# Optimization experiments

Hardware: AMD Instinct MI355X
Metric: run time of the kernel (lower is better)

The kernel has to match this reference:

```python
import jax, jax.numpy as jnp
from jax import lax
import numpy as np

B, C, S, H, DH, DV, DW = 16, 256, 64, 8, 32, 32, 32  # batch, channels, input_size, heads, d_h, d_v, d_w


def _dwconv(x, w, b):
    # depthwise 3x3 conv, stride 1, pad 1. w: [C,1,3,3]
    y = lax.conv_general_dilated(x, w, (1, 1), ((1, 1), (1, 1)),
                                 dimension_numbers=('NCHW', 'OIHW', 'NCHW'),
                                 feature_group_count=x.shape[1])
    return y + b[None, :, None, None]


def _linear(x, w, b):
    # torch Linear: w [out,in]
    return x @ w.T + b


def setup_inputs() -> dict:
    key = jax.random.key(0)
    ks = jax.random.split(key, 26)
    n = lambda k, shape, s=0.02: jax.random.normal(k, shape, jnp.float32) * s
    conv = lambda k: n(k, (C, 1, 3, 3), 0.1)
    return {
        'x': jax.random.normal(ks[0], (B, C, S, S), jnp.float32),
        'dw_qh_w': conv(ks[1]), 'dw_qh_b': n(ks[2], (C,)),
        'fc_qh_w': n(ks[3], (H * DH, C)), 'fc_qh_b': n(ks[4], (H * DH,)),
        'dw_kh_w': conv(ks[5]), 'dw_kh_b': n(ks[6], (C,)),
        'fc_kh_w': n(ks[7], (H * DH, C)), 'fc_kh_b': n(ks[8], (H * DH,)),
        'Bh': n(ks[9], (1, H, S, S)),
        'dw_v_w': conv(ks[10]), 'dw_v_b': n(ks[11], (C,)),
        'fc_v_w': n(ks[12], (H * DV, C)), 'fc_v_b': n(ks[13], (H * DV,)),
        'dw_qw_w': conv(ks[14]), 'dw_qw_b': n(ks[15], (C,)),
        'fc_qw_w': n(ks[16], (H * DW, C)), 'fc_qw_b': n(ks[17], (H * DW,)),
        'dw_kw_w': conv(ks[18]), 'dw_kw_b': n(ks[19], (C,)),
        'fc_kw_w': n(ks[20], (H * DW, C)), 'fc_kw_b': n(ks[21], (H * DW,)),
        'Bw': n(ks[22], (1, H, S, S)),
        'fc_o_w': n(ks[23], (C, H * DV)), 'fc_o_b': n(ks[24], (C,)),
    }


def reference(x, dw_qh_w, dw_qh_b, fc_qh_w, fc_qh_b,
              dw_kh_w, dw_kh_b, fc_kh_w, fc_kh_b, Bh,
              dw_v_w, dw_v_b, fc_v_w, fc_v_b,
              dw_qw_w, dw_qw_b, fc_qw_w, fc_qw_b,
              dw_kw_w, dw_kw_b, fc_kw_w, fc_kw_b, Bw,
              fc_o_w, fc_o_b):
    b, c, h, w = x.shape
    sh = DH ** -0.5
    sw = DW ** -0.5

    # height-axis queries/keys: dwconv -> adaptive avg pool over width -> linear
    qh = _dwconv(x, dw_qh_w, dw_qh_b).mean(axis=3).transpose(0, 2, 1)  # [b,h,c]
    qh = _linear(qh, fc_qh_w, fc_qh_b).reshape(b, h, H, DH).transpose(0, 2, 1, 3)  # [b,H,h,dh]
    kh = _dwconv(x, dw_kh_w, dw_kh_b).mean(axis=3).transpose(0, 2, 1)
    kh = _linear(kh, fc_kh_w, fc_kh_b).reshape(b, h, H, DH).transpose(0, 2, 1, 3)
    attn_h = jax.nn.softmax(jnp.einsum('bhid,bhjd->bhij', qh, kh) * sh + Bh, axis=-1)  # [b,H,h,h]

    # values over full HxW grid
    v = _dwconv(x, dw_v_w, dw_v_b).reshape(b, c, h * w).transpose(0, 2, 1)  # [b,hw,c]
    v = _linear(v, fc_v_w, fc_v_b).reshape(b, h, w, H, DV).transpose(0, 3, 1, 2, 4)  # [b,H,h,w,dv]
    v = v.reshape(b, H, h, w * DV)

    # width-axis queries/keys: dwconv -> adaptive avg pool over height -> linear
    qw = _dwconv(x, dw_qw_w, dw_qw_b).mean(axis=2).transpose(0, 2, 1)  # [b,w,c]
    qw = _linear(qw, fc_qw_w, fc_qw_b).reshape(b, w, H, DW).transpose(0, 2, 1, 3)  # [b,H,w,dw]
    kw = _dwconv(x, dw_kw_w, dw_kw_b).mean(axis=2).transpose(0, 2, 1)
    kw = _linear(kw, fc_kw_w, fc_kw_b).reshape(b, w, H, DW).transpose(0, 2, 1, 3)
    attn_w = jax.nn.softmax(jnp.einsum('bhid,bhjd->bhij', qw, kw) * sw + Bw, axis=-1)  # [b,H,w,w]

    # dual axial mixing: height attention, then width attention
    r = jnp.matmul(attn_h, v)                                # [b,H,h,w*dv]
    r = r.reshape(b, H, h, w, DV).transpose(0, 1, 2, 4, 3)    # [b,H,h,dv,w]
    r = r.reshape(b, H, h * DV, w)
    r = jnp.matmul(r, attn_w)                                # [b,H,h*dv,w]
    r = r.reshape(b, H, h, DV, w).transpose(0, 2, 4, 1, 3)    # [b,h,w,H,dv]
    r = r.reshape(b, h * w, H * DV)
    out = _linear(r, fc_o_w, fc_o_b).reshape(b, C, h, w)      # faithful to torch .view
    return out
```

## Files before the change

### kernel.cpp

```cpp
#include <hip/hip_runtime.h>
#include <hip/hip_bf16.h>

typedef float f4v __attribute__((ext_vector_type(4)));
typedef short s8v __attribute__((ext_vector_type(8)));
typedef unsigned short u8v __attribute__((ext_vector_type(8)));

__device__ __forceinline__ float bf2f(ushort u) {
  union { unsigned int i; float f; } c; c.i = ((unsigned int)u) << 16;
  return c.f;
}
__device__ __forceinline__ ushort f2bf(float f) {
  union { ushort s; __hip_bfloat16 h; } c; c.h = __float2bfloat16(f);
  return c.s;
}
__device__ __forceinline__ void gload16(const ushort* g, ushort* l) {
  __builtin_amdgcn_global_load_lds(
      (const __attribute__((address_space(1))) unsigned int*)g,
      (__attribute__((address_space(3))) unsigned int*)l, 16, 0, 0);
}

__global__ __launch_bounds__(256) void k_conv(
    const float* __restrict__ x,
    const float* __restrict__ wqh, const float* __restrict__ bqh,
    const float* __restrict__ wkh, const float* __restrict__ bkh,
    const float* __restrict__ wv,  const float* __restrict__ bv,
    const float* __restrict__ wqw, const float* __restrict__ bqw,
    const float* __restrict__ wkw, const float* __restrict__ bkw,
    const float* __restrict__ fq0, const float* __restrict__ fq1,
    const float* __restrict__ fq2, const float* __restrict__ fq3,
    const float* __restrict__ fwv, const float* __restrict__ fwo,
    ushort* __restrict__ whl, ushort* __restrict__ wbf,
    ushort* __restrict__ convV,
    float* __restrict__ qhm, float* __restrict__ khm,
    float* __restrict__ qwm, float* __restrict__ kwm) {
  __shared__ float xs[68 * 68];
  __shared__ float wl[5][9];
  __shared__ float bl[5];

  int bx = blockIdx.x;
  int tid = threadIdx.x;

  if (bx >= 4096) {
    int pb = bx - 4096;
    if (pb < 1024) {
      int mat = pb >> 8;
      int i = (pb & 255) * 256 + tid;
      const float* p = mat == 0 ? fq0 : mat == 1 ? fq1 : mat == 2 ? fq2 : fq3;
      float f = p[i];
      ushort hi = f2bf(f);
      ushort lo = f2bf(f - bf2f(hi));
      whl[(size_t)mat * 131072 + i] = hi;
      whl[(size_t)mat * 131072 + 65536 + i] = lo;
    } else {
      int idx = (pb - 1024) * 256 + tid;
      const float* src = (idx >> 16) ? fwo : fwv;
      wbf[idx] = f2bf(src[idx & 65535]);
    }
    return;
  }

  int b = bx >> 8;
  int c = bx & 255;
  int lane = tid & 63, wave = tid >> 6;

  const float* xp = x + (size_t)(b * 256 + c) * 4096;
#pragma unroll
  for (int i = 0; i < 4; i++) {
    int flat = tid + i * 256;
    int r = flat >> 4, c4 = (flat & 15) * 4;
    float4 v = *(const float4*)(xp + r * 64 + c4);
    *(float4*)&xs[(r + 1) * 68 + 4 + c4] = v;
  }
  if (tid < 72) { xs[tid] = 0.f; xs[65 * 68 + tid] = 0.f; }
  if (tid >= 72 && tid < 200) {
    int t = tid - 72;
    int pr = (t & 63) + 1, side = t >> 6;
    xs[pr * 68 + (side ? 68 : 3)] = 0.f;
  }
  if (tid >= 200 && tid < 245) {
    int t = tid - 200;
    int cw = t / 9, wi = t % 9;
    const float* wp = cw == 0 ? wqh : cw == 1 ? wkh : cw == 2 ? wv
                    : cw == 3 ? wqw : wkw;
    wl[cw][wi] = wp[c * 9 + wi];
  } else if (tid >= 245 && tid < 250) {
    int cw = tid - 245;
    const float* bp = cw == 0 ? bqh : cw == 1 ? bkh : cw == 2 ? bv
                    : cw == 3 ? bqw : bkw;
    bl[cw] = bp[c];
  }
  __syncthreads();

  {
    int w = lane;
    int h0 = wave * 16;
    float v0 = wl[2][0], v1 = wl[2][1], v2 = wl[2][2];
    float v3 = wl[2][3], v4 = wl[2][4], v5 = wl[2][5];
    float v6 = wl[2][6], v7 = wl[2][7], v8 = wl[2][8];
    float bvv = bl[2];
    float a00 = xs[h0 * 68 + 3 + w], a01 = xs[h0 * 68 + 4 + w],
          a02 = xs[h0 * 68 + 5 + w];
    float a10 = xs[(h0 + 1) * 68 + 3 + w], a11 = xs[(h0 + 1) * 68 + 4 + w],
          a12 = xs[(h0 + 1) * 68 + 5 + w];
    ushort* cp = convV + (size_t)(b * 256 + c) * 4096 + h0 * 64 + w;
#pragma unroll
    for (int i = 0; i < 16; i++) {
      int pr = h0 + i + 2;
      float a20 = xs[pr * 68 + 3 + w];
      float a21 = xs[pr * 68 + 4 + w];
      float a22 = xs[pr * 68 + 5 + w];
      float acc = bvv;
      acc += a00 * v0 + a01 * v1 + a02 * v2;
      acc += a10 * v3 + a11 * v4 + a12 * v5;
      acc += a20 * v6 + a21 * v7 + a22 * v8;
      cp[i * 64] = f2bf(acc);
      a00 = a10; a01 = a11; a02 = a12;
      a10 = a20; a11 = a21; a12 = a22;
    }
  }

  if (wave == 0) {
    float rs = 0.f, e0 = 0.f, e1 = 0.f;
    const float* rowp = &xs[(lane + 1) * 68 + 4];
#pragma unroll
    for (int i = 0; i < 16; i++) {
      float4 v = *(const float4*)(rowp + i * 4);
      rs += (v.x + v.y) + (v.z + v.w);
      if (i == 0) e0 = v.x;
      if (i == 15) e1 = v.w;
    }
    float rsP = __shfl(rs, lane - 1, 64); rsP = (lane == 0) ? 0.f : rsP;
    float rsN = __shfl(rs, lane + 1, 64); rsN = (lane == 63) ? 0.f : rsN;
    float e0P = __shfl(e0, lane - 1, 64); e0P = (lane == 0) ? 0.f : e0P;
    float e0N = __shfl(e0, lane + 1, 64); e0N = (lane == 63) ? 0.f : e0N;
    float e1P = __shfl(e1, lane - 1, 64); e1P = (lane == 0) ? 0.f : e1P;
    float e1N = __shfl(e1, lane + 1, 64); e1N = (lane == 63) ? 0.f : e1N;
    float RS[3] = {rsP, rs, rsN};
    float E0[3] = {e0P, e0, e0N};
    float E1[3] = {e1P, e1, e1N};
    float vq = 0.f, vk = 0.f;
#pragma unroll
    for (int ky = 0; ky < 3; ky++) {
      vq += (wl[0][ky * 3] + wl[0][ky * 3 + 1] + wl[0][ky * 3 + 2]) * RS[ky]
            - wl[0][ky * 3] * E1[ky] - wl[0][ky * 3 + 2] * E0[ky];
      vk += (wl[1][ky * 3] + wl[1][ky * 3 + 1] + wl[1][ky * 3 + 2]) * RS[ky]
            - wl[1][ky * 3] * E1[ky] - wl[1][ky * 3 + 2] * E0[ky];
    }
    qhm[(size_t)(b * 256 + c) * 64 + lane] = vq * (1.f / 64.f) + bl[0];
    khm[(size_t)(b * 256 + c) * 64 + lane] = vk * (1.f / 64.f) + bl[1];
  } else if (wave == 1) {
    float cs = 0.f, f0 = 0.f, f1 = 0.f;
#pragma unroll
    for (int r = 0; r < 64; r++) {
      float v = xs[(r + 1) * 68 + 4 + lane];
      cs += v;
      if (r == 0) f0 = v;
      if (r == 63) f1 = v;
    }
    float csP = __shfl(cs, lane - 1, 64); csP = (lane == 0) ? 0.f : csP;
    float csN = __shfl(cs, lane + 1, 64); csN = (lane == 63) ? 0.f : csN;
    float f0P = __shfl(f0, lane - 1, 64); f0P = (lane == 0) ? 0.f : f0P;
    float f0N = __shfl(f0, lane + 1, 64); f0N = (lane == 63) ? 0.f : f0N;
    float f1P = __shfl(f1, lane - 1, 64); f1P = (lane == 0) ? 0.f : f1P;
    float f1N = __shfl(f1, lane + 1, 64); f1N = (lane == 63) ? 0.f : f1N;
    float CS[3] = {csP, cs, csN};
    float F0[3] = {f0P, f0, f0N};
    float F1[3] = {f1P, f1, f1N};
    float vq = 0.f, vk = 0.f;
#pragma unroll
    for (int kx = 0; kx < 3; kx++) {
      vq += (wl[3][kx] + wl[3][3 + kx] + wl[3][6 + kx]) * CS[kx]
            - wl[3][kx] * F1[kx] - wl[3][6 + kx] * F0[kx];
      vk += (wl[4][kx] + wl[4][3 + kx] + wl[4][6 + kx]) * CS[kx]
            - wl[4][kx] * F1[kx] - wl[4][6 + kx] * F0[kx];
    }
    qwm[(size_t)(b * 256 + c) * 64 + lane] = vq * (1.f / 64.f) + bl[3];
    kwm[(size_t)(b * 256 + c) * 64 + lane] = vk * (1.f / 64.f) + bl[4];
  }
}

__global__ __launch_bounds__(256) void k_mmv(
    const ushort* __restrict__ A, const ushort* __restrict__ W,
    const float* __restrict__ bias, ushort* __restrict__ out,
    const float* __restrict__ s0, const float* __restrict__ s1,
    const float* __restrict__ s2, const float* __restrict__ s3,
    const ushort* __restrict__ whl,
    const float* __restrict__ b0, const float* __restrict__ b1,
    const float* __restrict__ b2, const float* __restrict__ b3,
    float* __restrict__ d0, float* __restrict__ d1,
    float* __restrict__ d2, float* __restrict__ d3) {
  __shared__ __align__(16) ushort pool[17408];

  int bx = blockIdx.x;
  int tid = threadIdx.x;
  int lane = tid & 63, wave = tid >> 6;
  int tm = lane & 15, quad = lane >> 4;

  if (bx < 512) {
    ushort* As = pool;
    ushort* Bs = pool + 4096;

    int m0 = bx * 128;
    int wm = (wave & 1) * 64, wn = (wave >> 1) * 128;
    int xorv = (tm ^ (tm >> 2)) & 3;
    int srow = lane >> 2;
    int slot = lane & 3;

    const ushort* Abase = A + (size_t)(m0 >> 12) * (256 * 4096) + (m0 & 4095);

    f4v acc[4][8] = {};

    for (int kc = 0; kc < 256; kc += 32) {
      __syncthreads();
      {
        int kr2 = (tid & 15) * 2, mg = tid >> 4;
        u8v v0 = *(const u8v*)&Abase[(size_t)(kc + kr2) * 4096 + mg * 8];
        u8v v1 = *(const u8v*)&Abase[(size_t)(kc + kr2 + 1) * 4096 + mg * 8];
        int sl0 = kr2 >> 3, k7 = kr2 & 7;
#pragma unroll
        for (int j = 0; j < 8; j++) {
          int row = mg * 8 + j;
          int xr = (row ^ (row >> 2)) & 3;
          ushort pr[2] = {v0[j], v1[j]};
          *(uint*)&As[row * 32 + (sl0 ^ xr) * 8 + k7] = *(uint*)pr;
        }
      }
#pragma unroll
      for (int it = 0; it < 4; it++) {
        int rb = wave * 16 + it * 64;
        int row = rb + srow;
        int xr = (row ^ (row >> 2)) & 3;
        gload16(&W[(size_t)row * 256 + kc + (slot ^ xr) * 8], &Bs[rb * 32]);
      }
      __syncthreads();

      s8v a[4];
#pragma unroll
      for (int mi = 0; mi < 4; mi++)
        a[mi] = *(const s8v*)&As[(wm + mi * 16 + tm) * 32 + (quad ^ xorv) * 8];
#pragma unroll
      for (int ni = 0; ni < 8; ni++) {
        s8v bfr =
            *(const s8v*)&Bs[(wn + ni * 16 + tm) * 32 + (quad ^ xorv) * 8];
#pragma unroll
        for (int mi = 0; mi < 4; mi++)
          acc[mi][ni] = __builtin_amdgcn_mfma_f32_16x16x32_bf16(
              a[mi], bfr, acc[mi][ni], 0, 0, 0);
      }
    }

#pragma unroll
    for (int mi = 0; mi < 4; mi++) {
#pragma unroll
      for (int ni = 0; ni < 8; ni++) {
        int col = wn + ni * 16 + tm;
        float bv = bias[col];
#pragma unroll
        for (int r = 0; r < 4; r++) {
          int row = m0 + wm + mi * 16 + quad * 4 + r;
          out[(size_t)row * 256 + col] = f2bf(acc[mi][ni][r] + bv);
        }
      }
    }
    return;
  }

  {
    int t = bx - 512;
    int z = t & 3;
    int n0 = ((t >> 2) & 3) * 64;
    int b = t >> 4;

    ushort* Ah = pool;
    ushort* Al = pool + 4352;
    ushort* Wh = pool + 8704;
    ushort* Wl = pool + 13056;

    const float* At = z == 0 ? s0 : z == 1 ? s1 : z == 2 ? s2 : s3;
    const ushort* Whp = whl + (size_t)z * 131072;
    const ushort* Wlp = Whp + 65536;
    const float* biasz = z == 0 ? b0 : z == 1 ? b1 : z == 2 ? b2 : b3;
    float* Cout = z == 0 ? d0 : z == 1 ? d1 : z == 2 ? d2 : d3;

    const float* Ab = At + (size_t)b * 256 * 64;

    int wm = (wave & 1) * 32, wn = (wave >> 1) * 32;

    f4v acc[2][2] = {};

    for (int kc = 0; kc < 256; kc += 64) {
      __syncthreads();
#pragma unroll
      for (int t2 = 0; t2 < 2; t2++) {
        int task = tid + t2 * 256;
        int mq = task & 15, kp = task >> 4;
        int k0 = kp * 2, m0 = mq * 4;
        float4 v0 = *(const float4*)&Ab[(size_t)(kc + k0) * 64 + m0];
        float4 v1 = *(const float4*)&Ab[(size_t)(kc + k0 + 1) * 64 + m0];
        float f0[4] = {v0.x, v0.y, v0.z, v0.w};
        float f1[4] = {v1.x, v1.y, v1.z, v1.w};
#pragma unroll
        for (int j = 0; j < 4; j++) {
          ushort h0 = f2bf(f0[j]), h1 = f2bf(f1[j]);
          ushort l0 = f2bf(f0[j] - bf2f(h0)), l1 = f2bf(f1[j] - bf2f(h1));
          ushort ph[2] = {h0, h1};
          ushort pl[2] = {l0, l1};
          *(uint*)&Ah[(m0 + j) * 68 + k0] = *(uint*)ph;
          *(uint*)&Al[(m0 + j) * 68 + k0] = *(uint*)pl;
        }
      }
#pragma unroll
      for (int t2 = 0; t2 < 2; t2++) {
        int task = tid + t2 * 256;
        int nr = task >> 3, k8 = (task & 7) * 8;
        *(u8v*)&Wh[nr * 68 + k8] =
            *(const u8v*)&Whp[(size_t)(n0 + nr) * 256 + kc + k8];
        *(u8v*)&Wl[nr * 68 + k8] =
            *(const u8v*)&Wlp[(size_t)(n0 + nr) * 256 + kc + k8];
      }
      __syncthreads();

#pragma unroll
      for (int ks = 0; ks < 64; ks += 32) {
        s8v ah[2], al[2], bh[2], bl[2];
#pragma unroll
        for (int mi = 0; mi < 2; mi++) {
          int idx = (wm + mi * 16 + tm) * 68 + ks + quad * 8;
          union { s8v v; unsigned long long u[2]; } th, tl;
          th.u[0] = *(const unsigned long long*)&Ah[idx];
          th.u[1] = *(const unsigned long long*)&Ah[idx + 4];
          tl.u[0] = *(const unsigned long long*)&Al[idx];
          tl.u[1] = *(const unsigned long long*)&Al[idx + 4];
          ah[mi] = th.v;
          al[mi] = tl.v;
        }
#pragma unroll
        for (int ni = 0; ni < 2; ni++) {
          int idx = (wn + ni * 16 + tm) * 68 + ks + quad * 8;
          union { s8v v; unsigned long long u[2]; } th, tl;
          th.u[0] = *(const unsigned long long*)&Wh[idx];
          th.u[1] = *(const unsigned long long*)&Wh[idx + 4];
          tl.u[0] = *(const unsigned long long*)&Wl[idx];
          tl.u[1] = *(const unsigned long long*)&Wl[idx + 4];
          bh[ni] = th.v;
          bl[ni] = tl.v;
        }
#pragma unroll
        for (int mi = 0; mi < 2; mi++)
#pragma unroll
          for (int ni = 0; ni < 2; ni++) {
            acc[mi][ni] = __builtin_amdgcn_mfma_f32_16x16x32_bf16(
                ah[mi], bh[ni], acc[mi][ni], 0, 0, 0);
            acc[mi][ni] = __builtin_amdgcn_mfma_f32_16x16x32_bf16(
                ah[mi], bl[ni], acc[mi][ni], 0, 0, 0);
            acc[mi][ni] = __builtin_amdgcn_mfma_f32_16x16x32_bf16(
                al[mi], bh[ni], acc[mi][ni], 0, 0, 0);
          }
      }
    }

#pragma unroll
    for (int mi = 0; mi < 2; mi++) {
#pragma unroll
      for (int ni = 0; ni < 2; ni++) {
        int n = n0 + wn + ni * 16 + tm;
        float bv = biasz[n];
#pragma unroll
        for (int r = 0; r < 4; r++) {
          int m = b * 64 + wm + mi * 16 + quad * 4 + r;
          Cout[(size_t)m * 256 + n] = acc[mi][ni][r] + bv;
        }
      }
    }
  }
}

template <int OUT_BF16, int AT>
__global__ __launch_bounds__(256) void k_mm(const ushort* __restrict__ A,
                                            const ushort* __restrict__ W,
                                            const float* __restrict__ bias,
                                            void* __restrict__ out) {
  __shared__ __align__(16) ushort As[128 * 32];
  __shared__ __align__(16) ushort Bs[128 * 32];

  int m0 = blockIdx.x * 128;
  int n0 = blockIdx.y * 128;
  int tid = threadIdx.x;
  int lane = tid & 63, wave = tid >> 6;
  int wm = (wave & 1) * 64, wn = (wave >> 1) * 64;
  int tm = lane & 15, quad = lane >> 4;
  int xorv = (tm ^ (tm >> 2)) & 3;
  int srow = lane >> 2;
  int slot = lane & 3;

  const ushort* Abase;
  if (AT) {
    Abase = A + (size_t)(m0 >> 12) * (256 * 4096) + (m0 & 4095);
  } else {
    Abase = A + (size_t)m0 * 256;
  }

  f4v acc[4][4] = {};

  for (int kc = 0; kc < 256; kc += 32) {
    __syncthreads();
    if (AT) {
      int kr2 = (tid & 15) * 2, mg = tid >> 4;
      u8v v0 = *(const u8v*)&Abase[(size_t)(kc + kr2) * 4096 + mg * 8];
      u8v v1 = *(const u8v*)&Abase[(size_t)(kc + kr2 + 1) * 4096 + mg * 8];
      int sl0 = kr2 >> 3, k7 = kr2 & 7;
#pragma unroll
      for (int j = 0; j < 8; j++) {
        int row = mg * 8 + j;
        int xr = (row ^ (row >> 2)) & 3;
        ushort pr[2] = {v0[j], v1[j]};
        *(uint*)&As[row * 32 + (sl0 ^ xr) * 8 + k7] = *(uint*)pr;
      }
#pragma unroll
      for (int it = 0; it < 2; it++) {
        int rb = wave * 16 + it * 64;
        int row = rb + srow;
        int xr = (row ^ (row >> 2)) & 3;
        gload16(&W[(size_t)(n0 + row) * 256 + kc + (slot ^ xr) * 8],
                &Bs[rb * 32]);
      }
    } else {
#pragma unroll
      for (int it = 0; it < 2; it++) {
        int rb = wave * 16 + it * 64;
        int row = rb + srow;
        int xr = (row ^ (row >> 2)) & 3;
        gload16(&Abase[(size_t)row * 256 + kc + (slot ^ xr) * 8],
                &As[rb * 32]);
        gload16(&W[(size_t)(n0 + row) * 256 + kc + (slot ^ xr) * 8],
                &Bs[rb * 32]);
      }
    }
    __syncthreads();

    s8v a[4], bfr[4];
#pragma unroll
    for (int mi = 0; mi < 4; mi++)
      a[mi] = *(const s8v*)&As[(wm + mi * 16 + tm) * 32 + (quad ^ xorv) * 8];
#pragma unroll
    for (int ni = 0; ni < 4; ni++)
      bfr[ni] = *(const s8v*)&Bs[(wn + ni * 16 + tm) * 32 + (quad ^ xorv) * 8];
#pragma unroll
    for (int mi = 0; mi < 4; mi++)
#pragma unroll
      for (int ni = 0; ni < 4; ni++)
        acc[mi][ni] = __builtin_amdgcn_mfma_f32_16x16x32_bf16(
            a[mi], bfr[ni], acc[mi][ni], 0, 0, 0);
  }

#pragma unroll
  for (int mi = 0; mi < 4; mi++) {
#pragma unroll
    for (int ni = 0; ni < 4; ni++) {
      int col = n0 + wn + ni * 16 + tm;
      float bv = bias[col];
#pragma unroll
      for (int r = 0; r < 4; r++) {
        int row = m0 + wm + mi * 16 + quad * 4 + r;
        float v = acc[mi][ni][r] + bv;
        if (OUT_BF16)
          ((ushort*)out)[(size_t)row * 256 + col] = f2bf(v);
        else
          ((float*)out)[(size_t)row * 256 + col] = v;
      }
    }
  }
}

__global__ __launch_bounds__(256) void k_attn(
    const float* __restrict__ qh, const float* __restrict__ kh,
    const float* __restrict__ Bh, float* __restrict__ ah,
    const float* __restrict__ qw, const float* __restrict__ kw,
    const float* __restrict__ Bw, float* __restrict__ aw, float scale) {
  __shared__ float qs[64 * 33];
  __shared__ float ks[64 * 33];

  int bx = blockIdx.x;
  int setw = bx >> 7;
  int rem = bx & 127;
  int hd = rem & 7, b = rem >> 3;
  int tid = threadIdx.x;
  int wave = tid >> 6, lane = tid & 63;

  const float* q = setw ? qw : qh;
  const float* k = setw ? kw : kh;
  const float* Bb = setw ? Bw : Bh;
  float* attn = setw ? aw : ah;

#pragma unroll
  for (int it = 0; it < 8; it++) {
    int f = tid + it * 256;
    int j = f >> 5, d = f & 31;
    size_t src = (size_t)(b * 64 + j) * 256 + hd * 32 + d;
    qs[j * 33 + d] = q[src];
    ks[j * 33 + d] = k[src];
  }
  __syncthreads();

  const float* Bp = Bb + (size_t)(hd * 64) * 64;
  float* ap = attn + (size_t)((b * 8 + hd) * 64) * 64;
  int j = lane;
  for (int ig = 0; ig < 16; ig++) {
    int i = ig * 4 + wave;
    float dot = 0.f;
#pragma unroll
    for (int d = 0; d < 32; d++) dot += qs[i * 33 + d] * ks[j * 33 + d];
    float logit = dot * scale + Bp[i * 64 + j];
    float mx = logit;
#pragma unroll
    for (int off = 32; off > 0; off >>= 1)
      mx = fmaxf(mx, __shfl_xor(mx, off, 64));
    float e = __expf(logit - mx);
    float sum = e;
#pragma unroll
    for (int off = 32; off > 0; off >>= 1) sum += __shfl_xor(sum, off, 64);
    ap[i * 64 + j] = e / sum;
  }
}

__global__ __launch_bounds__(256) void k_av(const float* __restrict__ attn,
                                            const ushort* __restrict__ vlin,
                                            ushort* __restrict__ r1) {
  __shared__ __align__(16) ushort Ah[64 * 68];
  __shared__ __align__(16) ushort Al[64 * 68];
  __shared__ __align__(16) ushort Bt[256 * 68];

  int bx = blockIdx.x;
  int nt = bx & 7, hd = (bx >> 3) & 7, b = bx >> 6;
  int n0 = nt * 256;
  int tid = threadIdx.x;
  int lane = tid & 63, wave = tid >> 6;

  const float* ap = attn + (size_t)(b * 8 + hd) * 4096;
  {
    int i = tid >> 2;
    int j0 = (tid & 3) * 16;
#pragma unroll
    for (int p = 0; p < 4; p++) {
      float4 v = *(const float4*)&ap[i * 64 + j0 + p * 4];
      float f_[4] = {v.x, v.y, v.z, v.w};
      ushort ph[4], pl[4];
#pragma unroll
      for (int q = 0; q < 4; q++) {
        ph[q] = f2bf(f_[q]);
        pl[q] = f2bf(f_[q] - bf2f(ph[q]));
      }
      *(uint2*)&Ah[i * 68 + j0 + p * 4] = *(uint2*)ph;
      *(uint2*)&Al[i * 68 + j0 + p * 4] = *(uint2*)pl;
    }
  }
  {
#pragma unroll
    for (int p = 0; p < 4; p++) {
      int task = tid + p * 256;
      int jp = task & 31;
      int cc = task >> 5;
      int j = jp * 2;
      int c = cc * 8;
      int gcol = n0 + c;
      int w = gcol >> 5, dv = gcol & 31;
      const ushort* vp =
          &vlin[(size_t)(b * 4096 + j * 64 + w) * 256 + hd * 32 + dv];
      u8v v0 = *(const u8v*)vp;
      u8v v1 = *(const u8v*)(vp + 64 * 256);
#pragma unroll
      for (int q = 0; q < 8; q++) {
        ushort pr[2] = {(ushort)v0[q], (ushort)v1[q]};
        *(uint*)&Bt[(c + q) * 68 + j] = *(uint*)pr;
      }
    }
  }
  __syncthreads();

  int tm = lane & 15, quad = lane >> 4;
  int wn = wave * 64;
  f4v acc[4][4] = {};
#pragma unroll
  for (int kc = 0; kc < 64; kc += 32) {
    s8v ah_[4], al_[4], bb[4];
#pragma unroll
    for (int mi = 0; mi < 4; mi++) {
      int idx = (mi * 16 + tm) * 68 + kc + quad * 8;
      union { s8v v; unsigned long long u[2]; } th, tl;
      th.u[0] = *(const unsigned long long*)&Ah[idx];
      th.u[1] = *(const unsigned long long*)&Ah[idx + 4];
      tl.u[0] = *(const unsigned long long*)&Al[idx];
      tl.u[1] = *(const unsigned long long*)&Al[idx + 4];
      ah_[mi] = th.v;
      al_[mi] = tl.v;
    }
#pragma unroll
    for (int ni = 0; ni < 4; ni++) {
      int idx = (wn + ni * 16 + tm) * 68 + kc + quad * 8;
      union { s8v v; unsigned long long u[2]; } tb;
      tb.u[0] = *(const unsigned long long*)&Bt[idx];
      tb.u[1] = *(const unsigned long long*)&Bt[idx + 4];
      bb[ni] = tb.v;
    }
#pragma unroll
    for (int mi = 0; mi < 4; mi++)
#pragma unroll
      for (int ni = 0; ni < 4; ni++) {
        acc[mi][ni] = __builtin_amdgcn_mfma_f32_16x16x32_bf16(
            ah_[mi], bb[ni], acc[mi][ni], 0, 0, 0);
        acc[mi][ni] = __builtin_amdgcn_mfma_f32_16x16x32_bf16(
            al_[mi], bb[ni], acc[mi][ni], 0, 0, 0);
      }
  }

  ushort* rp = r1 + (size_t)(b * 8 + hd) * 64 * 2048;
#pragma unroll
  for (int mi = 0; mi < 4; mi++) {
#pragma unroll
    for (int ni = 0; ni < 4; ni++) {
      int col = n0 + wn + ni * 16 + tm;
#pragma unroll
      for (int r = 0; r < 4; r++) {
        int row = mi * 16 + quad * 4 + r;
        rp[(size_t)row * 2048 + col] = f2bf(acc[mi][ni][r]);
      }
    }
  }
}

__global__ __launch_bounds__(256) void k_rw(const ushort* __restrict__ r1,
                                            const float* __restrict__ attnw,
                                            ushort* __restrict__ yT) {
  __shared__ __align__(16) ushort As[8 * 2180];
  __shared__ __align__(16) ushort Wh[64 * 68];
  __shared__ __align__(16) ushort Wl[64 * 68];

  int bx = blockIdx.x;
  int ht = bx & 7, hd = (bx >> 3) & 7, b = bx >> 6;
  int tid = threadIdx.x;
  int lane = tid & 63, wave = tid >> 6;

  {
    int h = tid >> 5;
    int t = tid & 31;
    const ushort* rp =
        r1 + (size_t)((b * 8 + hd) * 64 + ht * 8 + h) * 2048;
#pragma unroll
    for (int i = 0; i < 4; i++) {
      int chunk = t + 32 * i;
      int w = (chunk >> 2) * 2;
      int dv0 = (chunk & 3) * 8;
      u8v v0 = *(const u8v*)&rp[w * 32 + dv0];
      u8v v1 = *(const u8v*)&rp[(w + 1) * 32 + dv0];
#pragma unroll
      for (int j = 0; j < 8; j++) {
        ushort pr[2] = {(ushort)v0[j], (ushort)v1[j]};
        *(uint*)&As[h * 2180 + (dv0 + j) * 68 + w] = *(uint*)pr;
      }
    }
  }
  {
    const float* ap = attnw + (size_t)(b * 8 + hd) * 4096;
#pragma unroll
    for (int p = 0; p < 4; p++) {
      int w = (tid >> 4) + p * 16;
      int wq = (tid & 15) * 4;
      float4 v = *(const float4*)&ap[w * 64 + wq];
      float f_[4] = {v.x, v.y, v.z, v.w};
#pragma unroll
      for (int j = 0; j < 4; j++) {
        ushort hi = f2bf(f_[j]);
        Wh[(wq + j) * 68 + w] = hi;
        Wl[(wq + j) * 68 + w] = f2bf(f_[j] - bf2f(hi));
      }
    }
  }
  __syncthreads();

  int tm = lane & 15, quad = lane >> 4;
  int h0 = wave * 2;
  f4v acc[4][4] = {};
#pragma unroll
  for (int kc = 0; kc < 64; kc += 32) {
    s8v a[4], bh[4], bl[4];
#pragma unroll
    for (int mi = 0; mi < 4; mi++) {
      int h = h0 + (mi >> 1);
      int dv = (mi & 1) * 16 + tm;
      int idx = h * 2180 + dv * 68 + kc + quad * 8;
      union { s8v v; unsigned long long u[2]; } t_;
      t_.u[0] = *(const unsigned long long*)&As[idx];
      t_.u[1] = *(const unsigned long long*)&As[idx + 4];
      a[mi] = t_.v;
    }
#pragma unroll
    for (int ni = 0; ni < 4; ni++) {
      int idx = (ni * 16 + tm) * 68 + kc + quad * 8;
      union { s8v v; unsigned long long u[2]; } th, tl;
      th.u[0] = *(const unsigned long long*)&Wh[idx];
      th.u[1] = *(const unsigned long long*)&Wh[idx + 4];
      tl.u[0] = *(const unsigned long long*)&Wl[idx];
      tl.u[1] = *(const unsigned long long*)&Wl[idx + 4];
      bh[ni] = th.v;
      bl[ni] = tl.v;
    }
#pragma unroll
    for (int mi = 0; mi < 4; mi++)
#pragma unroll
      for (int ni = 0; ni < 4; ni++) {
        acc[mi][ni] = __builtin_amdgcn_mfma_f32_16x16x32_bf16(
            a[mi], bh[ni], acc[mi][ni], 0, 0, 0);
        acc[mi][ni] = __builtin_amdgcn_mfma_f32_16x16x32_bf16(
            a[mi], bl[ni], acc[mi][ni], 0, 0, 0);
      }
  }

#pragma unroll
  for (int mi = 0; mi < 4; mi++) {
    int h = ht * 8 + h0 + (mi >> 1);
    int dv0 = (mi & 1) * 16 + quad * 4;
#pragma unroll
    for (int ni = 0; ni < 4; ni++) {
      int wp = ni * 16 + tm;
      ushort pk[4];
#pragma unroll
      for (int r = 0; r < 4; r++) pk[r] = f2bf(acc[mi][ni][r]);
      *(uint2*)&yT[(size_t)(b * 4096 + h * 64 + wp) * 256 + hd * 32 + dv0] =
          *(uint2*)pk;
    }
  }
}

extern "C" void kernel_launch(void* const* d_in, const int* in_sizes, int n_in,
                              void* d_out, int out_size, void* d_ws,
                              size_t ws_size, hipStream_t stream) {
  const float* x      = (const float*)d_in[0];
  const float* dwqh_w = (const float*)d_in[1];
  const float* dwqh_b = (const float*)d_in[2];
  const float* fcqh_w = (const float*)d_in[3];
  const float* fcqh_b = (const float*)d_in[4];
  const float* dwkh_w = (const float*)d_in[5];
  const float* dwkh_b = (const float*)d_in[6];
  const float* fckh_w = (const float*)d_in[7];
  const float* fckh_b = (const float*)d_in[8];
  const float* Bh     = (const float*)d_in[9];
  const float* dwv_w  = (const float*)d_in[10];
  const float* dwv_b  = (const float*)d_in[11];
  const float* fcv_w  = (const float*)d_in[12];
  const float* fcv_b  = (const float*)d_in[13];
  const float* dwqw_w = (const float*)d_in[14];
  const float* dwqw_b = (const float*)d_in[15];
  const float* fcqw_w = (const float*)d_in[16];
  const float* fcqw_b = (const float*)d_in[17];
  const float* dwkw_w = (const float*)d_in[18];
  const float* dwkw_b = (const float*)d_in[19];
  const float* fckw_w = (const float*)d_in[20];
  const float* fckw_b = (const float*)d_in[21];
  const float* Bw     = (const float*)d_in[22];
  const float* fco_w  = (const float*)d_in[23];
  const float* fco_b  = (const float*)d_in[24];

  char* base = (char*)d_ws;
  ushort* P1 = (ushort*)(base);
  ushort* P2 = (ushort*)(base + 33554432);
  ushort* P3 = (ushort*)(base + 67108864);
  ushort* whl  = (ushort*)(base + 100663296);
  ushort* wv_bf = (ushort*)(base + 101711872);
  float* qhm = (float*)(base + 101974016);
  float* khm = qhm + 262144;
  float* qwm = khm + 262144;
  float* kwm = qwm + 262144;
  float* qhl = kwm + 262144;
  float* khl = qhl + 262144;
  float* qwl = khl + 262144;
  float* kwl = qwl + 262144;
  float* ah  = kwl + 262144;
  float* awt = ah + 524288;
  if (ws_size < 115000000ull) return;

  const float scale = 0.17677669529663687f;

  k_conv<<<5632, 256, 0, stream>>>(x, dwqh_w, dwqh_b, dwkh_w, dwkh_b, dwv_w,
                                   dwv_b, dwqw_w, dwqw_b, dwkw_w, dwkw_b,
                                   fcqh_w, fckh_w, fcqw_w, fckw_w, fcv_w,
                                   fco_w, whl, wv_bf, P1,
                                   qhm, khm, qwm, kwm);
  k_mmv<<<768, 256, 0, stream>>>(P1, wv_bf, fcv_b, P3,
                                 qhm, khm, qwm, kwm, whl, fcqh_b, fckh_b,
                                 fcqw_b, fckw_b, qhl, khl, qwl, kwl);
  k_attn<<<256, 256, 0, stream>>>(qhl, khl, Bh, ah, qwl, kwl, Bw, awt, scale);
  k_av<<<1024, 256, 0, stream>>>(ah, P3, P1);
  k_rw<<<1024, 256, 0, stream>>>(P1, awt, P2);
  k_mm<0, 0><<<dim3(512, 2), 256, 0, stream>>>(P2, wv_bf + 65536, fco_b, d_out);
}
```

Baseline: 273.1 us.

## Fuse attention softmax into AV and width-mix kernels; widen output GEMM tile

Removes the separate attention kernel and instead recomputes the 64x64 softmax attention maps inside each k_av and k_rw block, writing the hi/lo bf16 split directly to shared memory. This drops one launch and the global round trip of the attention matrices. In exchange, each of the 8 blocks per (batch, head) recomputes the same attention map redundantly. The output projection is also rewritten so each block covers all 256 output columns with a 128x256 tile, which halves the grid and reads the A tile once.

New measurement: 301.9 us. 10.5% more time.

```diff
diff --git a/kernel.cpp b/kernel.cpp
--- a/kernel.cpp
+++ b/kernel.cpp
@@ -375,157 +375,12 @@
   }
 }
 
-template <int OUT_BF16, int AT>
-__global__ __launch_bounds__(256) void k_mm(const ushort* __restrict__ A,
-                                            const ushort* __restrict__ W,
-                                            const float* __restrict__ bias,
-                                            void* __restrict__ out) {
-  __shared__ __align__(16) ushort As[128 * 32];
-  __shared__ __align__(16) ushort Bs[128 * 32];
-
-  int m0 = blockIdx.x * 128;
-  int n0 = blockIdx.y * 128;
-  int tid = threadIdx.x;
-  int lane = tid & 63, wave = tid >> 6;
-  int wm = (wave & 1) * 64, wn = (wave >> 1) * 64;
-  int tm = lane & 15, quad = lane >> 4;
-  int xorv = (tm ^ (tm >> 2)) & 3;
-  int srow = lane >> 2;
-  int slot = lane & 3;
-
-  const ushort* Abase;
-  if (AT) {
-    Abase = A + (size_t)(m0 >> 12) * (256 * 4096) + (m0 & 4095);
-  } else {
-    Abase = A + (size_t)m0 * 256;
-  }
-
-  f4v acc[4][4] = {};
-
-  for (int kc = 0; kc < 256; kc += 32) {
-    __syncthreads();
-    if (AT) {
-      int kr2 = (tid & 15) * 2, mg = tid >> 4;
-      u8v v0 = *(const u8v*)&Abase[(size_t)(kc + kr2) * 4096 + mg * 8];
-      u8v v1 = *(const u8v*)&Abase[(size_t)(kc + kr2 + 1) * 4096 + mg * 8];
-      int sl0 = kr2 >> 3, k7 = kr2 & 7;
-#pragma unroll
-      for (int j = 0; j < 8; j++) {
-        int row = mg * 8 + j;
-        int xr = (row ^ (row >> 2)) & 3;
-        ushort pr[2] = {v0[j], v1[j]};
-        *(uint*)&As[row * 32 + (sl0 ^ xr) * 8 + k7] = *(uint*)pr;
-      }
-#pragma unroll
-      for (int it = 0; it < 2; it++) {
-        int rb = wave * 16 + it * 64;
-        int row = rb + srow;
-        int xr = (row ^ (row >> 2)) & 3;
-        gload16(&W[(size_t)(n0 + row) * 256 + kc + (slot ^ xr) * 8],
-                &Bs[rb * 32]);
-      }
-    } else {
-#pragma unroll
-      for (int it = 0; it < 2; it++) {
-        int rb = wave * 16 + it * 64;
-        int row = rb + srow;
-        int xr = (row ^ (row >> 2)) & 3;
-        gload16(&Abase[(size_t)row * 256 + kc + (slot ^ xr) * 8],
-                &As[rb * 32]);
-        gload16(&W[(size_t)(n0 + row) * 256 + kc + (slot ^ xr) * 8],
-                &Bs[rb * 32]);
-      }
-    }
-    __syncthreads();
-
-    s8v a[4], bfr[4];
-#pragma unroll
-    for (int mi = 0; mi < 4; mi++)
-      a[mi] = *(const s8v*)&As[(wm + mi * 16 + tm) * 32 + (quad ^ xorv) * 8];
-#pragma unroll
-    for (int ni = 0; ni < 4; ni++)
-      bfr[ni] = *(const s8v*)&Bs[(wn + ni * 16 + tm) * 32 + (quad ^ xorv) * 8];
-#pragma unroll
-    for (int mi = 0; mi < 4; mi++)
-#pragma unroll
-      for (int ni = 0; ni < 4; ni++)
-        acc[mi][ni] = __builtin_amdgcn_mfma_f32_16x16x32_bf16(
-            a[mi], bfr[ni], acc[mi][ni], 0, 0, 0);
-  }
-
-#pragma unroll
-  for (int mi = 0; mi < 4; mi++) {
-#pragma unroll
-    for (int ni = 0; ni < 4; ni++) {
-      int col = n0 + wn + ni * 16 + tm;
-      float bv = bias[col];
-#pragma unroll
-      for (int r = 0; r < 4; r++) {
-        int row = m0 + wm + mi * 16 + quad * 4 + r;
-        float v = acc[mi][ni][r] + bv;
-        if (OUT_BF16)
-          ((ushort*)out)[(size_t)row * 256 + col] = f2bf(v);
-        else
-          ((float*)out)[(size_t)row * 256 + col] = v;
-      }
-    }
-  }
-}
-
-__global__ __launch_bounds__(256) void k_attn(
-    const float* __restrict__ qh, const float* __restrict__ kh,
-    const float* __restrict__ Bh, float* __restrict__ ah,
-    const float* __restrict__ qw, const float* __restrict__ kw,
-    const float* __restrict__ Bw, float* __restrict__ aw, float scale) {
-  __shared__ float qs[64 * 33];
-  __shared__ float ks[64 * 33];
-
-  int bx = blockIdx.x;
-  int setw = bx >> 7;
-  int rem = bx & 127;
-  int hd = rem & 7, b = rem >> 3;
-  int tid = threadIdx.x;
-  int wave = tid >> 6, lane = tid & 63;
-
-  const float* q = setw ? qw : qh;
-  const float* k = setw ? kw : kh;
-  const float* Bb = setw ? Bw : Bh;
-  float* attn = setw ? aw : ah;
-
-#pragma unroll
-  for (int it = 0; it < 8; it++) {
-    int f = tid + it * 256;
-    int j = f >> 5, d = f & 31;
-    size_t src = (size_t)(b * 64 + j) * 256 + hd * 32 + d;
-    qs[j * 33 + d] = q[src];
-    ks[j * 33 + d] = k[src];
-  }
-  __syncthreads();
-
-  const float* Bp = Bb + (size_t)(hd * 64) * 64;
-  float* ap = attn + (size_t)((b * 8 + hd) * 64) * 64;
-  int j = lane;
-  for (int ig = 0; ig < 16; ig++) {
-    int i = ig * 4 + wave;
-    float dot = 0.f;
-#pragma unroll
-    for (int d = 0; d < 32; d++) dot += qs[i * 33 + d] * ks[j * 33 + d];
-    float logit = dot * scale + Bp[i * 64 + j];
-    float mx = logit;
-#pragma unroll
-    for (int off = 32; off > 0; off >>= 1)
-      mx = fmaxf(mx, __shfl_xor(mx, off, 64));
-    float e = __expf(logit - mx);
-    float sum = e;
-#pragma unroll
-    for (int off = 32; off > 0; off >>= 1) sum += __shfl_xor(sum, off, 64);
-    ap[i * 64 + j] = e / sum;
-  }
-}
-
-__global__ __launch_bounds__(256) void k_av(const float* __restrict__ attn,
+__global__ __launch_bounds__(256) void k_av(const float* __restrict__ q,
+                                            const float* __restrict__ k,
+                                            const float* __restrict__ Bb,
                                             const ushort* __restrict__ vlin,
-                                            ushort* __restrict__ r1) {
+                                            ushort* __restrict__ r1,
+                                            float scale) {
   __shared__ __align__(16) ushort Ah[64 * 68];
   __shared__ __align__(16) ushort Al[64 * 68];
   __shared__ __align__(16) ushort Bt[256 * 68];
@@ -536,24 +391,42 @@
   int tid = threadIdx.x;
   int lane = tid & 63, wave = tid >> 6;
 
-  const float* ap = attn + (size_t)(b * 8 + hd) * 4096;
   {
-    int i = tid >> 2;
-    int j0 = (tid & 3) * 16;
-#pragma unroll
-    for (int p = 0; p < 4; p++) {
-      float4 v = *(const float4*)&ap[i * 64 + j0 + p * 4];
-      float f_[4] = {v.x, v.y, v.z, v.w};
-      ushort ph[4], pl[4];
-#pragma unroll
-      for (int q = 0; q < 4; q++) {
-        ph[q] = f2bf(f_[q]);
-        pl[q] = f2bf(f_[q] - bf2f(ph[q]));
-      }
-      *(uint2*)&Ah[i * 68 + j0 + p * 4] = *(uint2*)ph;
-      *(uint2*)&Al[i * 68 + j0 + p * 4] = *(uint2*)pl;
-    }
-  }
+    float* qs = (float*)Bt;
+    float* ks = qs + 64 * 33;
+#pragma unroll
+    for (int it = 0; it < 8; it++) {
+      int f = tid + it * 256;
+      int j = f >> 5, d = f & 31;
+      size_t src = (size_t)(b * 64 + j) * 256 + hd * 32 + d;
+      qs[j * 33 + d] = q[src];
+      ks[j * 33 + d] = k[src];
+    }
+    __syncthreads();
+    const float* Bp = Bb + (size_t)(hd * 64) * 64;
+    int j = lane;
+    for (int ig = 0; ig < 16; ig++) {
+      int i = ig * 4 + wave;
+      float dot = 0.f;
+#pragma unroll
+      for (int d = 0; d < 32; d++) dot += qs[i * 33 + d] * ks[j * 33 + d];
+      float logit = dot * scale + Bp[i * 64 + j];
+      float mx = logit;
+#pragma unroll
+      for (int off = 32; off > 0; off >>= 1)
+        mx = fmaxf(mx, __shfl_xor(mx, off, 64));
+      float e = __expf(logit - mx);
+      float sum = e;
+#pragma unroll
+      for (int off = 32; off > 0; off >>= 1) sum += __shfl_xor(sum, off, 64);
+      float a = e / sum;
+      ushort hi = f2bf(a);
+      Ah[i * 68 + j] = hi;
+      Al[i * 68 + j] = f2bf(a - bf2f(hi));
+    }
+    __syncthreads();
+  }
+
   {
 #pragma unroll
     for (int p = 0; p < 4; p++) {
@@ -569,9 +442,9 @@
       u8v v0 = *(const u8v*)vp;
       u8v v1 = *(const u8v*)(vp + 64 * 256);
 #pragma unroll
-      for (int q = 0; q < 8; q++) {
-        ushort pr[2] = {(ushort)v0[q], (ushort)v1[q]};
-        *(uint*)&Bt[(c + q) * 68 + j] = *(uint*)pr;
+      for (int qq = 0; qq < 8; qq++) {
+        ushort pr[2] = {(ushort)v0[qq], (ushort)v1[qq]};
+        *(uint*)&Bt[(c + qq) * 68 + j] = *(uint*)pr;
       }
     }
   }
@@ -629,8 +502,11 @@
 }
 
 __global__ __launch_bounds__(256) void k_rw(const ushort* __restrict__ r1,
-                                            const float* __restrict__ attnw,
-                                            ushort* __restrict__ yT) {
+                                            const float* __restrict__ q,
+                                            const float* __restrict__ k,
+                                            const float* __restrict__ Bb,
+                                            ushort* __restrict__ yT,
+                                            float scale) {
   __shared__ __align__(16) ushort As[8 * 2180];
   __shared__ __align__(16) ushort Wh[64 * 68];
   __shared__ __align__(16) ushort Wl[64 * 68];
@@ -639,6 +515,42 @@
   int ht = bx & 7, hd = (bx >> 3) & 7, b = bx >> 6;
   int tid = threadIdx.x;
   int lane = tid & 63, wave = tid >> 6;
+
+  {
+    float* qs = (float*)As;
+    float* ks = qs + 64 * 33;
+#pragma unroll
+    for (int it = 0; it < 8; it++) {
+      int f = tid + it * 256;
+      int j = f >> 5, d = f & 31;
+      size_t src = (size_t)(b * 64 + j) * 256 + hd * 32 + d;
+      qs[j * 33 + d] = q[src];
+      ks[j * 33 + d] = k[src];
+    }
+    __syncthreads();
+    const float* Bp = Bb + (size_t)(hd * 64) * 64;
+    int j = lane;
+    for (int ig = 0; ig < 16; ig++) {
+      int i = ig * 4 + wave;
+      float dot = 0.f;
+#pragma unroll
+      for (int d = 0; d < 32; d++) dot += qs[i * 33 + d] * ks[j * 33 + d];
+      float logit = dot * scale + Bp[i * 64 + j];
+      float mx = logit;
+#pragma unroll
+      for (int off = 32; off > 0; off >>= 1)
+        mx = fmaxf(mx, __shfl_xor(mx, off, 64));
+      float e = __expf(logit - mx);
+      float sum = e;
+#pragma unroll
+      for (int off = 32; off > 0; off >>= 1) sum += __shfl_xor(sum, off, 64);
+      float a = e / sum;
+      ushort hi = f2bf(a);
+      Wh[j * 68 + i] = hi;
+      Wl[j * 68 + i] = f2bf(a - bf2f(hi));
+    }
+    __syncthreads();
+  }
 
   {
     int h = tid >> 5;
@@ -656,22 +568,6 @@
       for (int j = 0; j < 8; j++) {
         ushort pr[2] = {(ushort)v0[j], (ushort)v1[j]};
         *(uint*)&As[h * 2180 + (dv0 + j) * 68 + w] = *(uint*)pr;
-      }
-    }
-  }
-  {
-    const float* ap = attnw + (size_t)(b * 8 + hd) * 4096;
-#pragma unroll
-    for (int p = 0; p < 4; p++) {
-      int w = (tid >> 4) + p * 16;
-      int wq = (tid & 15) * 4;
-      float4 v = *(const float4*)&ap[w * 64 + wq];
-      float f_[4] = {v.x, v.y, v.z, v.w};
-#pragma unroll
-      for (int j = 0; j < 4; j++) {
-        ushort hi = f2bf(f_[j]);
-        Wh[(wq + j) * 68 + w] = hi;
-        Wl[(wq + j) * 68 + w] = f2bf(f_[j] - bf2f(hi));
       }
     }
   }
@@ -727,6 +623,73 @@
       for (int r = 0; r < 4; r++) pk[r] = f2bf(acc[mi][ni][r]);
       *(uint2*)&yT[(size_t)(b * 4096 + h * 64 + wp) * 256 + hd * 32 + dv0] =
           *(uint2*)pk;
+    }
+  }
+}
+
+__global__ __launch_bounds__(256) void k_out(const ushort* __restrict__ A,
+                                             const ushort* __restrict__ W,
+                                             const float* __restrict__ bias,
+                                             float* __restrict__ out) {
+  __shared__ __align__(16) ushort As[128 * 32];
+  __shared__ __align__(16) ushort Bs[256 * 32];
+
+  int m0 = blockIdx.x * 128;
+  int tid = threadIdx.x;
+  int lane = tid & 63, wave = tid >> 6;
+  int wm = (wave & 1) * 64, wn = (wave >> 1) * 128;
+  int tm = lane & 15, quad = lane >> 4;
+  int xorv = (tm ^ (tm >> 2)) & 3;
+  int srow = lane >> 2;
+  int slot = lane & 3;
+
+  const ushort* Abase = A + (size_t)m0 * 256;
+
+  f4v acc[4][8] = {};
+
+  for (int kc = 0; kc < 256; kc += 32) {
+    __syncthreads();
+#pragma unroll
+    for (int it = 0; it < 2; it++) {
+      int rb = wave * 16 + it * 64;
+      int row = rb + srow;
+      int xr = (row ^ (row >> 2)) & 3;
+      gload16(&Abase[(size_t)row * 256 + kc + (slot ^ xr) * 8], &As[rb * 32]);
+    }
+#pragma unroll
+    for (int it = 0; it < 4; it++) {
+      int rb = wave * 16 + it * 64;
+      int row = rb + srow;
+      int xr = (row ^ (row >> 2)) & 3;
+      gload16(&W[(size_t)row * 256 + kc + (slot ^ xr) * 8], &Bs[rb * 32]);
+    }
+    __syncthreads();
+
+    s8v a[4];
+#pragma unroll
+    for (int mi = 0; mi < 4; mi++)
+      a[mi] = *(const s8v*)&As[(wm + mi * 16 + tm) * 32 + (quad ^ xorv) * 8];
+#pragma unroll
+    for (int ni = 0; ni < 8; ni++) {
+      s8v bfr = *(const s8v*)&Bs[(wn + ni * 16 + tm) * 32 + (quad ^ xorv) * 8];
+#pragma unroll
+      for (int mi = 0; mi < 4; mi++)
+        acc[mi][ni] = __builtin_amdgcn_mfma_f32_16x16x32_bf16(
+            a[mi], bfr, acc[mi][ni], 0, 0, 0);
+    }
+  }
+
+#pragma unroll
+  for (int mi = 0; mi < 4; mi++) {
+#pragma unroll
+    for (int ni = 0; ni < 8; ni++) {
+      int col = wn + ni * 16 + tm;
+      float bv = bias[col];
+#pragma unroll
+      for (int r = 0; r < 4; r++) {
+        int row = m0 + wm + mi * 16 + quad * 4 + r;
+        out[(size_t)row * 256 + col] = acc[mi][ni][r] + bv;
+      }
     }
   }
 }
@@ -774,8 +737,6 @@
   float* khl = qhl + 262144;
   float* qwl = khl + 262144;
   float* kwl = qwl + 262144;
-  float* ah  = kwl + 262144;
-  float* awt = ah + 524288;
   if (ws_size < 115000000ull) return;
 
   const float scale = 0.17677669529663687f;
@@ -788,8 +749,7 @@
   k_mmv<<<768, 256, 0, stream>>>(P1, wv_bf, fcv_b, P3,
                                  qhm, khm, qwm, kwm, whl, fcqh_b, fckh_b,
                                  fcqw_b, fckw_b, qhl, khl, qwl, kwl);
-  k_attn<<<256, 256, 0, stream>>>(qhl, khl, Bh, ah, qwl, kwl, Bw, awt, scale);
-  k_av<<<1024, 256, 0, stream>>>(ah, P3, P1);
-  k_rw<<<1024, 256, 0, stream>>>(P1, awt, P2);
-  k_mm<0, 0><<<dim3(512, 2), 256, 0, stream>>>(P2, wv_bf + 65536, fco_b, d_out);
-}
+  k_av<<<1024, 256, 0, stream>>>(qhl, khl, Bh, P3, P1, scale);
+  k_rw<<<1024, 256, 0, stream>>>(P1, qwl, kwl, Bw, P2, scale);
+  k_out<<<512, 256, 0, stream>>>(P2, wv_bf + 65536, fco_b, (float*)d_out);
+}
```
